# Kernel optimization log

Measured on AMD Instinct MI355X. Metric: run time of the kernel, lower is better.

Reference implementation:

```python
import jax, jax.numpy as jnp
import numpy as np
from jax import lax

IN_CH, OUT_CH, KS, GROUPS = 64, 64, 3, 8
FPG = IN_CH // GROUPS  # features per group = 8
PAD = KS // 2


def setup_inputs() -> dict:
    key = jax.random.key(0)
    k1, k2, k3 = jax.random.split(key, 3)
    x = jax.random.normal(k1, (8, IN_CH, 256, 256), dtype=jnp.float32)
    representation = jax.random.normal(k2, (8, 32), dtype=jnp.float32)
    # Linear(32, OUT_CH*KS*KS, bias=False) weight, torch layout (out_features, in_features)
    W = jax.random.normal(k3, (OUT_CH * KS * KS, 32), dtype=jnp.float32) * (1.0 / np.sqrt(32))
    return {"x": x, "representation": representation, "W": W}


def reference(x, representation, W):
    b = x.shape[0]
    # ReflectionPad2d
    xp = jnp.pad(x, ((0, 0), (0, 0), (PAD, PAD), (PAD, PAD)), mode="reflect")
    # compress_key: Linear (no bias) + LeakyReLU(0.1)
    k = jax.nn.leaky_relu(representation @ W.T, 0.1)  # [b, OUT_CH*KS*KS]
    kernel = k.reshape(b, OUT_CH, 1, KS, KS)
    # repeat_interleave on a size-1 dim == broadcast/tile
    kernel = jnp.broadcast_to(kernel, (b, OUT_CH, FPG, KS, KS))
    # per-sample grouped conv (equivalent to torch's batch-as-groups trick)
    def conv_one(xi, ki):
        # xi: [C,H,W], ki: [OUT_CH, FPG, KS, KS]
        out = lax.conv_general_dilated(
            xi[None], ki, window_strides=(1, 1), padding="VALID",
            dimension_numbers=("NCHW", "OIHW", "NCHW"),
            feature_group_count=GROUPS)
        return out[0]
    return jax.vmap(conv_one)(xp, kernel)  # [b, OUT_CH, H, W]
```

## Files before the change

kernel.cpp:

```cpp
#include <hip/hip_runtime.h>


#define TH 32
#define TW 64
#define LDSW 68

__device__ __forceinline__ int reflect1(int i, int n) {
  if (i < 0) i = -i;
  if (i >= n) i = 2 * n - 2 - i;
  return i;
}

__global__ __launch_bounds__(256) void dynconv_kernel(
    const float* __restrict__ x,
    const float* __restrict__ rep,
    const float* __restrict__ W,
    float* __restrict__ out) {
  const int tid = threadIdx.x;
  const int tx = blockIdx.x & 3;
  const int ty = (blockIdx.x >> 2) & 7;
  const int g  = (blockIdx.x >> 5) & 7;
  const int b  = blockIdx.x >> 8;

  __shared__ float s[(TH + 2) * LDSW];
  __shared__ float wl[72];

  if (tid < 72) {
    const int row = g * 72 + tid;
    const float* wr = W + (size_t)row * 32;
    const float* rb = rep + b * 32;
    float acc = 0.f;
#pragma unroll
    for (int j = 0; j < 32; ++j) acc += rb[j] * wr[j];
    wl[tid] = (acc > 0.f) ? acc : 0.1f * acc;
  }
  __syncthreads();

  const int gx0 = tx * TW, gy0 = ty * TH;
  const float* xg = x + ((size_t)(b * 64 + g * 8)) * 65536;
  const float4* xg4 = (const float4*)xg;

  for (int t = tid; t < 34 * 16; t += 256) {
    const int row = t >> 4, seg = t & 15;
    const int yy = reflect1(gy0 + row - 1, 256);
    const float4* p = xg4 + (size_t)yy * 64 + (gx0 >> 2) + seg;
    float4 a; a.x = 0.f; a.y = 0.f; a.z = 0.f; a.w = 0.f;
#pragma unroll
    for (int c = 0; c < 8; ++c) {
      float4 v = p[(size_t)c * 16384];
      a.x += v.x; a.y += v.y; a.z += v.z; a.w += v.w;
    }
    *(float4*)&s[row * LDSW + seg * 4] = a;
  }
  if (tid < 68) {
    const int row = tid >> 1, side = tid & 1;
    const int scol = side ? 64 : 66;
    const int yy = reflect1(gy0 + row - 1, 256);
    const int xx = reflect1(gx0 + (side ? 64 : -1), 256);
    const float* p = xg + (size_t)yy * 256 + xx;
    float a = 0.f;
#pragma unroll
    for (int c = 0; c < 8; ++c) a += p[(size_t)c * 65536];
    s[row * LDSW + scol] = a;
  }
  __syncthreads();

  const int cs = (tid & 15) * 4;
  const int r0 = tid >> 4;

  for (int rr = r0; rr < TH; rr += 16) {
    float win[3][6];
#pragma unroll
    for (int dy = 0; dy < 3; ++dy) {
#pragma unroll
      for (int dx = 0; dx < 6; ++dx) {
        const int col = cs - 1 + dx;
        const int scol = (col < 0) ? 66 : col;
        win[dy][dx] = s[(rr + dy) * LDSW + scol];
      }
    }

    const int y = gy0 + rr;
    float* ob = out + (((size_t)(b * 64 + g * 8) * 256 + y) * 256 + gx0 + cs);

#pragma unroll
    for (int oc = 0; oc < 8; ++oc) {
      const float* w = &wl[oc * 9];
      const float w00 = w[0], w01 = w[1], w02 = w[2];
      const float w10 = w[3], w11 = w[4], w12 = w[5];
      const float w20 = w[6], w21 = w[7], w22 = w[8];
      float4 o;
      o.x = w00 * win[0][0] + w01 * win[0][1] + w02 * win[0][2]
          + w10 * win[1][0] + w11 * win[1][1] + w12 * win[1][2]
          + w20 * win[2][0] + w21 * win[2][1] + w22 * win[2][2];
      o.y = w00 * win[0][1] + w01 * win[0][2] + w02 * win[0][3]
          + w10 * win[1][1] + w11 * win[1][2] + w12 * win[1][3]
          + w20 * win[2][1] + w21 * win[2][2] + w22 * win[2][3];
      o.z = w00 * win[0][2] + w01 * win[0][3] + w02 * win[0][4]
          + w10 * win[1][2] + w11 * win[1][3] + w12 * win[1][4]
          + w20 * win[2][2] + w21 * win[2][3] + w22 * win[2][4];
      o.w = w00 * win[0][3] + w01 * win[0][4] + w02 * win[0][5]
          + w10 * win[1][3] + w11 * win[1][4] + w12 * win[1][5]
          + w20 * win[2][3] + w21 * win[2][4] + w22 * win[2][5];
      *(float4*)(ob + (size_t)oc * 65536) = o;
    }
  }
}

extern "C" void kernel_launch(void* const* d_in, const int* in_sizes, int n_in,
                              void* d_out, int out_size, void* d_ws, size_t ws_size,
                              hipStream_t stream) {
  const float* x   = (const float*)d_in[0];
  const float* rep = (const float*)d_in[1];
  const float* W   = (const float*)d_in[2];
  float* out = (float*)d_out;
  hipLaunchKernelGGL(dynconv_kernel, dim3(2048), dim3(256), 0, stream,
                     x, rep, W, out);
}
```

Before: 251.0 us.

## Split group channel-sum into separate pass, then conv from summed planes

The input channels of each group are first reduced into a workspace buffer by a streaming kernel. A second kernel then runs the 3x3 conv from that buffer with 16-row tiles, twice as many blocks, and vectorised LDS window loads. This is meant to remove the halo re-reads of all 8 channels and give a simpler, better-overlapped streaming pattern. In exchange it adds an extra launch and a 16 MB write plus read of the intermediate, and falls back to the fused kernel when the workspace is too small.

```diff
diff --git a/kernel.cpp b/kernel.cpp
--- a/kernel.cpp
+++ b/kernel.cpp
@@ -1,8 +1,6 @@
 #include <hip/hip_runtime.h>
 
 
-#define TH 32
-#define TW 64
 #define LDSW 68
 
 __device__ __forceinline__ int reflect1(int i, int n) {
@@ -11,18 +9,38 @@
   return i;
 }
 
-__global__ __launch_bounds__(256) void dynconv_kernel(
+__global__ __launch_bounds__(256) void gsum_kernel(
     const float* __restrict__ x,
+    float* __restrict__ S) {
+  const int i = blockIdx.x * 256 + threadIdx.x;
+  const int plane = i >> 14;
+  const int off = i & 16383;
+  const float4* p = (const float4*)x + (size_t)plane * 8 * 16384 + off;
+  float4 a;
+  {
+    float4 v0 = p[0],         v1 = p[16384],     v2 = p[2 * 16384], v3 = p[3 * 16384];
+    float4 v4 = p[4 * 16384], v5 = p[5 * 16384], v6 = p[6 * 16384], v7 = p[7 * 16384];
+    a.x = ((v0.x + v1.x) + (v2.x + v3.x)) + ((v4.x + v5.x) + (v6.x + v7.x));
+    a.y = ((v0.y + v1.y) + (v2.y + v3.y)) + ((v4.y + v5.y) + (v6.y + v7.y));
+    a.z = ((v0.z + v1.z) + (v2.z + v3.z)) + ((v4.z + v5.z) + (v6.z + v7.z));
+    a.w = ((v0.w + v1.w) + (v2.w + v3.w)) + ((v4.w + v5.w) + (v6.w + v7.w));
+  }
+  ((float4*)S)[i] = a;
+}
+
+#define BTH 16
+__global__ __launch_bounds__(256) void dynconv3_kernel(
+    const float* __restrict__ S,
     const float* __restrict__ rep,
     const float* __restrict__ W,
     float* __restrict__ out) {
   const int tid = threadIdx.x;
   const int tx = blockIdx.x & 3;
-  const int ty = (blockIdx.x >> 2) & 7;
-  const int g  = (blockIdx.x >> 5) & 7;
-  const int b  = blockIdx.x >> 8;
-
-  __shared__ float s[(TH + 2) * LDSW];
+  const int ty = (blockIdx.x >> 2) & 15;
+  const int g  = (blockIdx.x >> 6) & 7;
+  const int b  = blockIdx.x >> 9;
+
+  __shared__ float s[(BTH + 2) * LDSW];
   __shared__ float wl[72];
 
   if (tid < 72) {
@@ -34,6 +52,89 @@
     for (int j = 0; j < 32; ++j) acc += rb[j] * wr[j];
     wl[tid] = (acc > 0.f) ? acc : 0.1f * acc;
   }
+
+  const int gx0 = tx * 64, gy0 = ty * BTH;
+  const float* Sp = S + (size_t)(b * 8 + g) * 65536;
+  const float4* Sp4 = (const float4*)Sp;
+
+  for (int t = tid; t < 18 * 16; t += 256) {
+    const int row = t >> 4, seg = t & 15;
+    const int yy = reflect1(gy0 + row - 1, 256);
+    float4 v = Sp4[(size_t)yy * 64 + (gx0 >> 2) + seg];
+    *(float4*)&s[row * LDSW + seg * 4] = v;
+  }
+  if (tid < 36) {
+    const int row = tid >> 1, side = tid & 1;
+    const int scol = side ? 64 : 66;
+    const int yy = reflect1(gy0 + row - 1, 256);
+    const int xx = reflect1(gx0 + (side ? 64 : -1), 256);
+    s[row * LDSW + scol] = Sp[(size_t)yy * 256 + xx];
+  }
+  __syncthreads();
+
+  const int cs = (tid & 15) * 4;
+  const int rr = tid >> 4;
+
+  float win[3][6];
+#pragma unroll
+  for (int dy = 0; dy < 3; ++dy) {
+    const float* row = &s[(rr + dy) * LDSW];
+    float4 a = *(const float4*)&row[cs];
+    float  r = row[cs + 4];
+    float  l = row[(cs == 0) ? 66 : cs - 1];
+    win[dy][0] = l;   win[dy][1] = a.x; win[dy][2] = a.y;
+    win[dy][3] = a.z; win[dy][4] = a.w; win[dy][5] = r;
+  }
+
+  const int y = gy0 + rr;
+  float* ob = out + (((size_t)(b * 64 + g * 8) * 256 + y) * 256 + gx0 + cs);
+
+#pragma unroll
+  for (int oc = 0; oc < 8; ++oc) {
+    const float* w = &wl[oc * 9];
+    const float w00 = w[0], w01 = w[1], w02 = w[2];
+    const float w10 = w[3], w11 = w[4], w12 = w[5];
+    const float w20 = w[6], w21 = w[7], w22 = w[8];
+    float4 o;
+    o.x = w00 * win[0][0] + w01 * win[0][1] + w02 * win[0][2]
+        + w10 * win[1][0] + w11 * win[1][1] + w12 * win[1][2]
+        + w20 * win[2][0] + w21 * win[2][1] + w22 * win[2][2];
+    o.y = w00 * win[0][1] + w01 * win[0][2] + w02 * win[0][3]
+        + w10 * win[1][1] + w11 * win[1][2] + w12 * win[1][3]
+        + w20 * win[2][1] + w21 * win[2][2] + w22 * win[2][3];
+    o.z = w00 * win[0][2] + w01 * win[0][3] + w02 * win[0][4]
+        + w10 * win[1][2] + w11 * win[1][3] + w12 * win[1][4]
+        + w20 * win[2][2] + w21 * win[2][3] + w22 * win[2][4];
+    o.w = w00 * win[0][3] + w01 * win[0][4] + w02 * win[0][5]
+        + w10 * win[1][3] + w11 * win[1][4] + w12 * win[1][5]
+        + w20 * win[2][3] + w21 * win[2][4] + w22 * win[2][5];
+    *(float4*)(ob + (size_t)oc * 65536) = o;
+  }
+}
+
+#define TH 32
+#define TW 64
+__global__ __launch_bounds__(256) void dynconv_fused_kernel(
+    const float* __restrict__ x, const float* __restrict__ rep,
+    const float* __restrict__ W, float* __restrict__ out) {
+  const int tid = threadIdx.x;
+  const int tx = blockIdx.x & 3;
+  const int ty = (blockIdx.x >> 2) & 7;
+  const int g  = (blockIdx.x >> 5) & 7;
+  const int b  = blockIdx.x >> 8;
+
+  __shared__ float s[(TH + 2) * LDSW];
+  __shared__ float wl[72];
+
+  if (tid < 72) {
+    const int row = g * 72 + tid;
+    const float* wr = W + (size_t)row * 32;
+    const float* rb = rep + b * 32;
+    float acc = 0.f;
+#pragma unroll
+    for (int j = 0; j < 32; ++j) acc += rb[j] * wr[j];
+    wl[tid] = (acc > 0.f) ? acc : 0.1f * acc;
+  }
   __syncthreads();
 
   const int gx0 = tx * TW, gy0 = ty * TH;
@@ -67,22 +168,19 @@
 
   const int cs = (tid & 15) * 4;
   const int r0 = tid >> 4;
-
   for (int rr = r0; rr < TH; rr += 16) {
     float win[3][6];
 #pragma unroll
     for (int dy = 0; dy < 3; ++dy) {
-#pragma unroll
-      for (int dx = 0; dx < 6; ++dx) {
-        const int col = cs - 1 + dx;
-        const int scol = (col < 0) ? 66 : col;
-        win[dy][dx] = s[(rr + dy) * LDSW + scol];
-      }
+      const float* row = &s[(rr + dy) * LDSW];
+      float4 a = *(const float4*)&row[cs];
+      float  r = row[cs + 4];
+      float  l = row[(cs == 0) ? 66 : cs - 1];
+      win[dy][0] = l;   win[dy][1] = a.x; win[dy][2] = a.y;
+      win[dy][3] = a.z; win[dy][4] = a.w; win[dy][5] = r;
     }
-
     const int y = gy0 + rr;
     float* ob = out + (((size_t)(b * 64 + g * 8) * 256 + y) * 256 + gx0 + cs);
-
 #pragma unroll
     for (int oc = 0; oc < 8; ++oc) {
       const float* w = &wl[oc * 9];
@@ -114,6 +212,15 @@
   const float* rep = (const float*)d_in[1];
   const float* W   = (const float*)d_in[2];
   float* out = (float*)d_out;
-  hipLaunchKernelGGL(dynconv_kernel, dim3(2048), dim3(256), 0, stream,
-                     x, rep, W, out);
-}
+
+  const size_t s_bytes = (size_t)8 * 8 * 256 * 256 * sizeof(float);
+  if (ws_size >= s_bytes) {
+    float* S = (float*)d_ws;
+    hipLaunchKernelGGL(gsum_kernel, dim3(4096), dim3(256), 0, stream, x, S);
+    hipLaunchKernelGGL(dynconv3_kernel, dim3(4096), dim3(256), 0, stream,
+                       S, rep, W, out);
+  } else {
+    hipLaunchKernelGGL(dynconv_fused_kernel, dim3(2048), dim3(256), 0, stream,
+                       x, rep, W, out);
+  }
+}
```

New measurement: 247.0 us. No clear change (-1.6%).
